# Optimization experiments

Measured on AMD Instinct MI355X. Metric: run time of the kernel, lower is better.

The kernel has to match this reference:

```python
import jax, jax.numpy as jnp
import numpy as np

N_NODES = 50000
N_EDGES = 500000
H_DIM = 128
OUT_DIM = 16
N_RELS = 90
N_BASES = 4


def setup_inputs() -> dict:
    key = jax.random.key(0)
    ks = jax.random.split(key, 12)
    inp = {
        'node_ids': jnp.arange(N_NODES, dtype=jnp.int32),
        'src': jax.random.randint(ks[0], (N_EDGES,), 0, N_NODES, dtype=jnp.int32),
        'dst': jax.random.randint(ks[1], (N_EDGES,), 0, N_NODES, dtype=jnp.int32),
        'etype': jax.random.randint(ks[2], (N_EDGES,), 0, N_RELS, dtype=jnp.int32),
        'emb': jax.random.normal(ks[3], (N_NODES, H_DIM), jnp.float32),
        'basis1': jax.random.normal(ks[4], (N_BASES, H_DIM, H_DIM), jnp.float32) * (1.0 / np.sqrt(H_DIM)),
        'comp1': jax.random.normal(ks[5], (N_RELS, N_BASES), jnp.float32) * (1.0 / np.sqrt(N_BASES)),
        'loop_w1': jax.random.normal(ks[6], (H_DIM, H_DIM), jnp.float32) * (1.0 / np.sqrt(H_DIM)),
        'bias1': jnp.zeros((H_DIM,), jnp.float32),
        'basis2': jax.random.normal(ks[7], (N_BASES, H_DIM, OUT_DIM), jnp.float32) * (1.0 / np.sqrt(H_DIM)),
        'comp2': jax.random.normal(ks[8], (N_RELS, N_BASES), jnp.float32) * (1.0 / np.sqrt(N_BASES)),
        'loop_w2': jax.random.normal(ks[9], (H_DIM, OUT_DIM), jnp.float32) * (1.0 / np.sqrt(H_DIM)),
        'bias2': jnp.zeros((OUT_DIM,), jnp.float32),
    }
    return inp


def _rel_graph_conv(x, src, dst, etype, basis, comp, loop_w, bias, num_nodes):
    # Basis decomposition: W_r = sum_b comp[r,b] * basis[b].
    # Project node features through each basis first (N is smaller than E),
    # then combine per-edge with relation coefficients: avoids per-edge GEMM.
    xb = jnp.einsum('ni,bio->nbo', x, basis)            # [N, B, out]
    msg = jnp.einsum('eb,ebo->eo', comp[etype], xb[src])  # [E, out]
    agg = jax.ops.segment_sum(msg, dst, num_segments=num_nodes)  # [N, out]
    # apply_norm=True: divide aggregated messages by in-degree of dst.
    deg = jax.ops.segment_sum(jnp.ones((src.shape[0],), x.dtype), dst,
                              num_segments=num_nodes)
    h = agg * (1.0 / jnp.maximum(deg, 1.0))[:, None]
    # self_loop=True plus bias.
    return h + x @ loop_w + bias


def reference(node_ids, src, dst, etype, emb, basis1, comp1, loop_w1, bias1,
              basis2, comp2, loop_w2, bias2):
    n = emb.shape[0]
    x = emb[node_ids]                                   # embedding lookup
    h = jax.nn.relu(_rel_graph_conv(x, src, dst, etype, basis1, comp1,
                                    loop_w1, bias1, n))
    out = _rel_graph_conv(h, src, dst, etype, basis2, comp2, loop_w2, bias2, n)
    return out
```

## Files before the change

kernel.cpp:

```cpp
#include <hip/hip_runtime.h>
#include <hip/hip_bf16.h>

#define N_NODES 50000
#define N_EDGES 500000
#define H_DIM 128
#define OUT_DIM 16
#define KDIM 640

typedef short short8 __attribute__((ext_vector_type(8)));
typedef float f32x4 __attribute__((ext_vector_type(4)));
typedef float f32x2 __attribute__((ext_vector_type(2)));

__device__ inline unsigned short f2b(float f) {
  unsigned u = __float_as_uint(f);
  u += 0x7fffu + ((u >> 16) & 1u);
  return (unsigned short)(u >> 16);
}
__device__ inline float b2f(unsigned short u) {
  return __uint_as_float(((unsigned)u) << 16);
}

__device__ __forceinline__ void gload_lds16(const unsigned short* g, unsigned short* l) {
  __builtin_amdgcn_global_load_lds(
      (const __attribute__((address_space(1))) unsigned int*)g,
      (__attribute__((address_space(3))) unsigned int*)l, 16, 0, 0);
}

#define CONV_BLOCKS 6250
#define PREP_BLOCKS 360
#define INIT_BLOCKS 196
__global__ void prologue_kernel(const int* __restrict__ node_ids, const float* __restrict__ emb,
                                unsigned short* __restrict__ Abuf,
                                const float* __restrict__ basis1, const float* __restrict__ loop_w1,
                                const float* __restrict__ basis2, const float* __restrict__ loop_w2,
                                unsigned short* __restrict__ B1t, unsigned short* __restrict__ B2pt,
                                int* __restrict__ cntA, int* __restrict__ cntB,
                                int* __restrict__ counter) {
  int b = blockIdx.x;
  if (b < CONV_BLOCKS) {
    int tid = b * 256 + threadIdx.x;
    if (tid >= N_NODES * (H_DIM / 4)) return;
    int n = tid >> 5;
    int q = tid & 31;
    int id = node_ids[n];
    const float4 v = *reinterpret_cast<const float4*>(emb + (size_t)id * H_DIM + q * 4);
    uint2 p;
    p.x = (unsigned)f2b(v.x) | ((unsigned)f2b(v.y) << 16);
    p.y = (unsigned)f2b(v.z) | ((unsigned)f2b(v.w) << 16);
    *reinterpret_cast<uint2*>(Abuf + (size_t)n * KDIM + 512 + q * 4) = p;
  } else if (b < CONV_BLOCKS + PREP_BLOCKS) {
    int tid = (b - CONV_BLOCKS) * 256 + threadIdx.x;
    if (tid < 128 * KDIM) {
      int c = tid / KDIM, k = tid % KDIM;
      float v = (k < 512) ? basis1[k * 128 + c] : loop_w1[(k - 512) * 128 + c];
      B1t[c * KDIM + k] = f2b(v);
    } else if (tid < 128 * KDIM + 80 * 128) {
      int t2 = tid - 128 * KDIM;
      int c = t2 / 128, k = t2 % 128;
      float v = (c < 64) ? basis2[(c >> 4) * 128 * 16 + k * 16 + (c & 15)]
                         : loop_w2[k * 16 + (c - 64)];
      B2pt[c * 128 + k] = f2b(v);
    }
  } else {
    int i = (b - CONV_BLOCKS - PREP_BLOCKS) * 256 + threadIdx.x;
    if (i < N_NODES) {
      cntA[i] = 0;
      cntB[i] = 0;
    }
    if (i == 0) *counter = 0;
  }
}

__global__ void count_kernel(const int* __restrict__ dst, int* __restrict__ cnt) {
  for (int e = blockIdx.x * blockDim.x + threadIdx.x; e < N_EDGES; e += gridDim.x * blockDim.x)
    atomicAdd(&cnt[dst[e]], 1);
}

__global__ void alloc_kernel(const int* __restrict__ cnt, int* __restrict__ start,
                             int* __restrict__ counter) {
  int i = blockIdx.x * blockDim.x + threadIdx.x;
  int lane = threadIdx.x & 63;
  int c = (i < N_NODES) ? cnt[i] : 0;
  int incl = c;
#pragma unroll
  for (int off = 1; off < 64; off <<= 1) {
    int v = __shfl_up(incl, off, 64);
    if (lane >= off) incl += v;
  }
  int waveTotal = __shfl(incl, 63, 64);
  int base = 0;
  if (lane == 63) base = atomicAdd(counter, waveTotal);
  base = __shfl(base, 63, 64);
  if (i < N_NODES) start[i] = base + incl - c;
}

__global__ void fill_kernel(const int* __restrict__ src, const int* __restrict__ dst,
                            const int* __restrict__ et, const int* __restrict__ csr_start,
                            int* __restrict__ cnt, unsigned* __restrict__ csr_se) {
  for (int e = blockIdx.x * blockDim.x + threadIdx.x; e < N_EDGES; e += gridDim.x * blockDim.x) {
    int d = dst[e];
    int idx = csr_start[d] + atomicAdd(&cnt[d], 1);
    csr_se[idx] = (unsigned)src[e] | ((unsigned)et[e] << 16);
  }
}

__global__ __launch_bounds__(256) void agg_kernel(const int* __restrict__ csr_start,
                                                  const int* __restrict__ csr_cnt,
                                                  const unsigned* __restrict__ csr_se,
                                                  const float* __restrict__ comp,
                                                  unsigned short* __restrict__ Abuf) {
  int node = blockIdx.x * 4 + (threadIdx.x >> 6);
  if (node >= N_NODES) return;
  int lane = threadIdx.x & 63;
  int lo = __builtin_amdgcn_readfirstlane(csr_start[node]);
  int deg = __builtin_amdgcn_readfirstlane(csr_cnt[node]);
  int hi = lo + deg;

  f32x2 a0 = {0.f, 0.f}, a1 = {0.f, 0.f}, a2 = {0.f, 0.f}, a3 = {0.f, 0.f};
  const unsigned short* featb = Abuf + 512;
  const int laneoff = lane * 2;

#define EDGE_BODY(J)                                                                   \
  {                                                                                    \
    unsigned v = __builtin_amdgcn_readlane(myse, (J));                                 \
    int s = (int)(v & 0xFFFFu);                                                        \
    int t = (int)(v >> 16);                                                            \
    unsigned u = *reinterpret_cast<const unsigned*>(featb + s * KDIM + laneoff);       \
    float4 c = *reinterpret_cast<const float4*>(comp + t * 4);                         \
    f32x2 x;                                                                           \
    x.x = __uint_as_float(u << 16);                                                    \
    x.y = __uint_as_float(u & 0xffff0000u);                                            \
    a0 = __builtin_elementwise_fma((f32x2){c.x, c.x}, x, a0);                          \
    a1 = __builtin_elementwise_fma((f32x2){c.y, c.y}, x, a1);                          \
    a2 = __builtin_elementwise_fma((f32x2){c.z, c.z}, x, a2);                          \
    a3 = __builtin_elementwise_fma((f32x2){c.w, c.w}, x, a3);                          \
  }

  for (int e0 = lo; e0 < hi; e0 += 64) {
    int nchunk = min(hi - e0, 64);
    unsigned myse = 0;
    if (e0 + lane < hi) myse = csr_se[e0 + lane];
    int j = 0;
    for (; j + 8 <= nchunk; j += 8) {
      EDGE_BODY(j)
      EDGE_BODY(j + 1)
      EDGE_BODY(j + 2)
      EDGE_BODY(j + 3)
      EDGE_BODY(j + 4)
      EDGE_BODY(j + 5)
      EDGE_BODY(j + 6)
      EDGE_BODY(j + 7)
    }
    if (j + 4 <= nchunk) {
      EDGE_BODY(j)
      EDGE_BODY(j + 1)
      EDGE_BODY(j + 2)
      EDGE_BODY(j + 3)
      j += 4;
    }
    for (; j < nchunk; ++j) { EDGE_BODY(j) }
  }
#undef EDGE_BODY

  float inv = 1.0f / (float)(deg > 0 ? deg : 1);
  unsigned short* out = Abuf + (size_t)node * KDIM;
  unsigned p0w = (unsigned)f2b(a0.x * inv) | ((unsigned)f2b(a0.y * inv) << 16);
  unsigned p1w = (unsigned)f2b(a1.x * inv) | ((unsigned)f2b(a1.y * inv) << 16);
  unsigned p2w = (unsigned)f2b(a2.x * inv) | ((unsigned)f2b(a2.y * inv) << 16);
  unsigned p3w = (unsigned)f2b(a3.x * inv) | ((unsigned)f2b(a3.y * inv) << 16);
  *reinterpret_cast<unsigned*>(out + 0 * 128 + laneoff) = p0w;
  *reinterpret_cast<unsigned*>(out + 1 * 128 + laneoff) = p1w;
  *reinterpret_cast<unsigned*>(out + 2 * 128 + laneoff) = p2w;
  *reinterpret_cast<unsigned*>(out + 3 * 128 + laneoff) = p3w;
}

__global__ __launch_bounds__(256) void agg2_kernel(const int* __restrict__ csr_start,
                                                   const int* __restrict__ csr_cnt,
                                                   const unsigned* __restrict__ csr_se,
                                                   const float* __restrict__ comp,
                                                   const unsigned short* __restrict__ Abuf,
                                                   const float* __restrict__ bias2,
                                                   float* __restrict__ dout) {
  int node = blockIdx.x * 4 + (threadIdx.x >> 6);
  if (node >= N_NODES) return;
  int lane = threadIdx.x & 63;
  int bsel = lane >> 4;
  int o = lane & 15;
  int lo = __builtin_amdgcn_readfirstlane(csr_start[node]);
  int deg = __builtin_amdgcn_readfirstlane(csr_cnt[node]);
  int hi = lo + deg;

  float acc = 0.f;

#define EDGE2_BODY(J)                                                      \
  {                                                                        \
    unsigned v = __builtin_amdgcn_readlane(myse, (J));                     \
    int s = (int)(v & 0xFFFFu);                                            \
    int t = (int)(v >> 16);                                                \
    unsigned short u = Abuf[s * KDIM + lane];                              \
    float4 c = *reinterpret_cast<const float4*>(comp + t * 4);             \
    float cb = (bsel < 2) ? ((bsel == 0) ? c.x : c.y)                      \
                          : ((bsel == 2) ? c.z : c.w);                     \
    acc = fmaf(cb, b2f(u), acc);                                           \
  }

  for (int e0 = lo; e0 < hi; e0 += 64) {
    int nchunk = min(hi - e0, 64);
    unsigned myse = 0;
    if (e0 + lane < hi) myse = csr_se[e0 + lane];
    int j = 0;
    for (; j + 8 <= nchunk; j += 8) {
      EDGE2_BODY(j)
      EDGE2_BODY(j + 1)
      EDGE2_BODY(j + 2)
      EDGE2_BODY(j + 3)
      EDGE2_BODY(j + 4)
      EDGE2_BODY(j + 5)
      EDGE2_BODY(j + 6)
      EDGE2_BODY(j + 7)
    }
    if (j + 4 <= nchunk) {
      EDGE2_BODY(j)
      EDGE2_BODY(j + 1)
      EDGE2_BODY(j + 2)
      EDGE2_BODY(j + 3)
      j += 4;
    }
    for (; j < nchunk; ++j) { EDGE2_BODY(j) }
  }
#undef EDGE2_BODY

  acc += __shfl_xor(acc, 16, 64);
  acc += __shfl_xor(acc, 32, 64);

  if (lane < 16) {
    float inv = 1.0f / (float)(deg > 0 ? deg : 1);
    float sl = b2f(Abuf[(size_t)node * KDIM + 64 + o]);
    dout[(size_t)node * OUT_DIM + o] = acc * inv + sl + bias2[o];
  }
}

__global__ __launch_bounds__(256) void gemm1p_kernel(const unsigned short* __restrict__ A,
                                                     const unsigned short* __restrict__ B1t,
                                                     const float* __restrict__ bias1,
                                                     const unsigned short* __restrict__ B2pt,
                                                     unsigned short* __restrict__ Abuf, int M) {
  __shared__ unsigned short As[64][64];
  __shared__ unsigned short Bs[128][64];
  __shared__ unsigned short Hs[64][128];
  int wave = threadIdx.x >> 6;
  int lane = threadIdx.x & 63;
  int row0 = blockIdx.x * 64;
  int kh = lane >> 4;
  int cl = lane & 15;
  int ar = wave * 16 + cl;
  f32x4 acc[8] = {};

  for (int k0 = 0; k0 < KDIM; k0 += 64) {
#pragma unroll
    for (int p = 0; p < 2; ++p) {
      int cid = threadIdx.x + p * 256;
      int r = cid >> 3, c8 = cid & 7;
      int gr = row0 + r;
      gload_lds16(A + (size_t)gr * KDIM + k0 + ((c8 ^ (r & 7)) * 8), &As[0][0] + cid * 8);
    }
#pragma unroll
    for (int p = 0; p < 4; ++p) {
      int cid = threadIdx.x + p * 256;
      int r = cid >> 3, c8 = cid & 7;
      gload_lds16(B1t + (size_t)r * KDIM + k0 + ((c8 ^ (r & 7)) * 8), &Bs[0][0] + cid * 8);
    }
    __syncthreads();
    short8 a0 = *reinterpret_cast<const short8*>(&As[ar][((kh) ^ (ar & 7)) * 8]);
    short8 a1 = *reinterpret_cast<const short8*>(&As[ar][((4 + kh) ^ (ar & 7)) * 8]);
#pragma unroll
    for (int ct = 0; ct < 8; ++ct) {
      int bc = ct * 16 + cl;
      short8 b0 = *reinterpret_cast<const short8*>(&Bs[bc][((kh) ^ (bc & 7)) * 8]);
      short8 b1 = *reinterpret_cast<const short8*>(&Bs[bc][((4 + kh) ^ (bc & 7)) * 8]);
      acc[ct] = __builtin_amdgcn_mfma_f32_16x16x32_bf16(a0, b0, acc[ct], 0, 0, 0);
      acc[ct] = __builtin_amdgcn_mfma_f32_16x16x32_bf16(a1, b1, acc[ct], 0, 0, 0);
    }
    __syncthreads();
  }

  int rb = wave * 16 + (lane >> 4) * 4;
#pragma unroll
  for (int ct = 0; ct < 8; ++ct) {
    int col = ct * 16 + cl;
    float bv = bias1[col];
#pragma unroll
    for (int r = 0; r < 4; ++r) {
      int lr = rb + r;
      float v = fmaxf(acc[ct][r] + bv, 0.0f);
      unsigned short hb = f2b(v);
      int c8 = col >> 3;
      int c8s = (c8 & 8) | ((c8 ^ lr) & 7);
      *reinterpret_cast<unsigned short*>(
          reinterpret_cast<char*>(&Hs[lr][0]) + c8s * 16 + (col & 7) * 2) = hb;
    }
  }
  __syncthreads();

  f32x4 acc2[5] = {};
  for (int k0 = 0; k0 < 128; k0 += 64) {
    for (int cid = threadIdx.x; cid < 80 * 8; cid += 256) {
      int r = cid >> 3, c8 = cid & 7;
      short8 v = *reinterpret_cast<const short8*>(B2pt + r * 128 + k0 + c8 * 8);
      *reinterpret_cast<short8*>(&Bs[r][(c8 ^ (r & 7)) * 8]) = v;
    }
    __syncthreads();
    int c8a = (k0 >> 3) + kh;
    int c8b = (k0 >> 3) + 4 + kh;
    short8 a0 = *reinterpret_cast<const short8*>(
        reinterpret_cast<char*>(&Hs[ar][0]) + (((c8a ^ ar) & 7) | (c8a & 8)) * 16);
    short8 a1 = *reinterpret_cast<const short8*>(
        reinterpret_cast<char*>(&Hs[ar][0]) + (((c8b ^ ar) & 7) | (c8b & 8)) * 16);
#pragma unroll
    for (int ct = 0; ct < 5; ++ct) {
      int bc = ct * 16 + cl;
      short8 b0 = *reinterpret_cast<const short8*>(&Bs[bc][((kh) ^ (bc & 7)) * 8]);
      short8 b1 = *reinterpret_cast<const short8*>(&Bs[bc][((4 + kh) ^ (bc & 7)) * 8]);
      acc2[ct] = __builtin_amdgcn_mfma_f32_16x16x32_bf16(a0, b0, acc2[ct], 0, 0, 0);
      acc2[ct] = __builtin_amdgcn_mfma_f32_16x16x32_bf16(a1, b1, acc2[ct], 0, 0, 0);
    }
    __syncthreads();
  }

#pragma unroll
  for (int ct = 0; ct < 5; ++ct) {
    int col = ct * 16 + cl;
#pragma unroll
    for (int r = 0; r < 4; ++r) {
      int gr = row0 + rb + r;
      if (gr < M) Abuf[(size_t)gr * KDIM + col] = f2b(acc2[ct][r]);
    }
  }
}

extern "C" void kernel_launch(void* const* d_in, const int* in_sizes, int n_in,
                              void* d_out, int out_size, void* d_ws, size_t ws_size,
                              hipStream_t stream) {
  const int* node_ids = (const int*)d_in[0];
  const int* src = (const int*)d_in[1];
  const int* dst = (const int*)d_in[2];
  const int* etype = (const int*)d_in[3];
  const float* emb = (const float*)d_in[4];
  const float* basis1 = (const float*)d_in[5];
  const float* comp1 = (const float*)d_in[6];
  const float* loop_w1 = (const float*)d_in[7];
  const float* bias1 = (const float*)d_in[8];
  const float* basis2 = (const float*)d_in[9];
  const float* comp2 = (const float*)d_in[10];
  const float* loop_w2 = (const float*)d_in[11];
  const float* bias2 = (const float*)d_in[12];
  (void)in_sizes; (void)n_in; (void)out_size; (void)ws_size;

  char* ws = (char*)d_ws;
  size_t off = 0;
  auto alloc = [&](size_t bytes) -> void* {
    void* p = ws + off;
    off += (bytes + 255) & ~(size_t)255;
    return p;
  };
  int* csr_start = (int*)alloc(N_NODES * sizeof(int));
  int* cntA = (int*)alloc(N_NODES * sizeof(int));
  int* cntB = (int*)alloc(N_NODES * sizeof(int));
  int* counter = (int*)alloc(sizeof(int));
  unsigned* csr_se = (unsigned*)alloc((size_t)N_EDGES * sizeof(unsigned));
  unsigned short* Abuf = (unsigned short*)alloc((size_t)N_NODES * KDIM * sizeof(unsigned short));
  unsigned short* B1t = (unsigned short*)alloc(128 * KDIM * sizeof(unsigned short));
  unsigned short* B2pt = (unsigned short*)alloc(80 * 128 * sizeof(unsigned short));

  prologue_kernel<<<CONV_BLOCKS + PREP_BLOCKS + INIT_BLOCKS, 256, 0, stream>>>(
      node_ids, emb, Abuf, basis1, loop_w1, basis2, loop_w2, B1t, B2pt, cntA, cntB, counter);
  count_kernel<<<1024, 256, 0, stream>>>(dst, cntA);
  alloc_kernel<<<(N_NODES + 255) / 256, 256, 0, stream>>>(cntA, csr_start, counter);
  fill_kernel<<<1024, 256, 0, stream>>>(src, dst, etype, csr_start, cntB, csr_se);

  agg_kernel<<<(N_NODES + 3) / 4, 256, 0, stream>>>(csr_start, cntA, csr_se, comp1, Abuf);
  gemm1p_kernel<<<(N_NODES + 63) / 64, 256, 0, stream>>>(Abuf, B1t, bias1, B2pt, Abuf, N_NODES);

  agg2_kernel<<<(N_NODES + 3) / 4, 256, 0, stream>>>(csr_start, cntA, csr_se, comp2, Abuf,
                                                     bias2, (float*)d_out);
}
```

Before: 146.8 us.

## Process two nodes per wave in aggregation and double-buffer GEMM LDS tiles

Both aggregation kernels now give each wavefront two consecutive destination nodes. They load the CSR start and count as int2 and prefetch the first edge chunk for both nodes up front, so the edge-record loads of the second node overlap with work on the first. The fused GEMM kernel now uses a double-buffered LDS layout: it issues async global-to-LDS loads for the next K tile while MFMAs run on the current one, and reuses one shared buffer for Hs and the second-stage B tile. The cost is fewer waves in the aggregation kernels, which gives less latency hiding across waves, and a larger LDS footprint per block in the GEMM, which may lower occupancy.

New measurement: 149.2 us. Within noise of the previous version (+1.6%).

```diff
diff --git a/kernel.cpp b/kernel.cpp
--- a/kernel.cpp
+++ b/kernel.cpp
@@ -109,14 +109,19 @@
                                                   const unsigned* __restrict__ csr_se,
                                                   const float* __restrict__ comp,
                                                   unsigned short* __restrict__ Abuf) {
-  int node = blockIdx.x * 4 + (threadIdx.x >> 6);
-  if (node >= N_NODES) return;
+  int pair = blockIdx.x * 4 + (threadIdx.x >> 6);
+  int nodeA = pair * 2;
+  if (nodeA >= N_NODES) return;
   int lane = threadIdx.x & 63;
-  int lo = __builtin_amdgcn_readfirstlane(csr_start[node]);
-  int deg = __builtin_amdgcn_readfirstlane(csr_cnt[node]);
-  int hi = lo + deg;
-
-  f32x2 a0 = {0.f, 0.f}, a1 = {0.f, 0.f}, a2 = {0.f, 0.f}, a3 = {0.f, 0.f};
+  int2 st2 = *reinterpret_cast<const int2*>(csr_start + nodeA);
+  int2 ct2 = *reinterpret_cast<const int2*>(csr_cnt + nodeA);
+  int loA = __builtin_amdgcn_readfirstlane(st2.x);
+  int degA = __builtin_amdgcn_readfirstlane(ct2.x);
+  int loB = __builtin_amdgcn_readfirstlane(st2.y);
+  int degB = __builtin_amdgcn_readfirstlane(ct2.y);
+  unsigned recA = (lane < degA) ? csr_se[loA + lane] : 0;
+  unsigned recB = (lane < degB) ? csr_se[loB + lane] : 0;
+
   const unsigned short* featb = Abuf + 512;
   const int laneoff = lane * 2;
 
@@ -136,42 +141,41 @@
     a3 = __builtin_elementwise_fma((f32x2){c.w, c.w}, x, a3);                          \
   }
 
-  for (int e0 = lo; e0 < hi; e0 += 64) {
-    int nchunk = min(hi - e0, 64);
-    unsigned myse = 0;
-    if (e0 + lane < hi) myse = csr_se[e0 + lane];
-    int j = 0;
-    for (; j + 8 <= nchunk; j += 8) {
-      EDGE_BODY(j)
-      EDGE_BODY(j + 1)
-      EDGE_BODY(j + 2)
-      EDGE_BODY(j + 3)
-      EDGE_BODY(j + 4)
-      EDGE_BODY(j + 5)
-      EDGE_BODY(j + 6)
-      EDGE_BODY(j + 7)
-    }
-    if (j + 4 <= nchunk) {
-      EDGE_BODY(j)
-      EDGE_BODY(j + 1)
-      EDGE_BODY(j + 2)
-      EDGE_BODY(j + 3)
-      j += 4;
-    }
-    for (; j < nchunk; ++j) { EDGE_BODY(j) }
-  }
+#define PROCESS1(NODE, LO, DEG, REC0)                                                  \
+  {                                                                                    \
+    f32x2 a0 = {0.f, 0.f}, a1 = {0.f, 0.f}, a2 = {0.f, 0.f}, a3 = {0.f, 0.f};          \
+    int hi = (LO) + (DEG);                                                             \
+    unsigned myse = (REC0);                                                            \
+    for (int e0 = (LO); e0 < hi; e0 += 64) {                                           \
+      int nchunk = min(hi - e0, 64);                                                   \
+      if (e0 != (LO)) myse = (e0 + lane < hi) ? csr_se[e0 + lane] : 0;                 \
+      int j = 0;                                                                       \
+      for (; j + 8 <= nchunk; j += 8) {                                                \
+        EDGE_BODY(j) EDGE_BODY(j + 1) EDGE_BODY(j + 2) EDGE_BODY(j + 3)                \
+        EDGE_BODY(j + 4) EDGE_BODY(j + 5) EDGE_BODY(j + 6) EDGE_BODY(j + 7)            \
+      }                                                                                \
+      if (j + 4 <= nchunk) {                                                           \
+        EDGE_BODY(j) EDGE_BODY(j + 1) EDGE_BODY(j + 2) EDGE_BODY(j + 3)                \
+        j += 4;                                                                        \
+      }                                                                                \
+      for (; j < nchunk; ++j) { EDGE_BODY(j) }                                         \
+    }                                                                                  \
+    float inv = 1.0f / (float)((DEG) > 0 ? (DEG) : 1);                                 \
+    unsigned short* out = Abuf + (size_t)(NODE)*KDIM;                                  \
+    unsigned p0w = (unsigned)f2b(a0.x * inv) | ((unsigned)f2b(a0.y * inv) << 16);      \
+    unsigned p1w = (unsigned)f2b(a1.x * inv) | ((unsigned)f2b(a1.y * inv) << 16);      \
+    unsigned p2w = (unsigned)f2b(a2.x * inv) | ((unsigned)f2b(a2.y * inv) << 16);      \
+    unsigned p3w = (unsigned)f2b(a3.x * inv) | ((unsigned)f2b(a3.y * inv) << 16);      \
+    *reinterpret_cast<unsigned*>(out + 0 * 128 + laneoff) = p0w;                       \
+    *reinterpret_cast<unsigned*>(out + 1 * 128 + laneoff) = p1w;                       \
+    *reinterpret_cast<unsigned*>(out + 2 * 128 + laneoff) = p2w;                       \
+    *reinterpret_cast<unsigned*>(out + 3 * 128 + laneoff) = p3w;                       \
+  }
+
+  PROCESS1(nodeA, loA, degA, recA)
+  PROCESS1(nodeA + 1, loB, degB, recB)
+#undef PROCESS1
 #undef EDGE_BODY
-
-  float inv = 1.0f / (float)(deg > 0 ? deg : 1);
-  unsigned short* out = Abuf + (size_t)node * KDIM;
-  unsigned p0w = (unsigned)f2b(a0.x * inv) | ((unsigned)f2b(a0.y * inv) << 16);
-  unsigned p1w = (unsigned)f2b(a1.x * inv) | ((unsigned)f2b(a1.y * inv) << 16);
-  unsigned p2w = (unsigned)f2b(a2.x * inv) | ((unsigned)f2b(a2.y * inv) << 16);
-  unsigned p3w = (unsigned)f2b(a3.x * inv) | ((unsigned)f2b(a3.y * inv) << 16);
-  *reinterpret_cast<unsigned*>(out + 0 * 128 + laneoff) = p0w;
-  *reinterpret_cast<unsigned*>(out + 1 * 128 + laneoff) = p1w;
-  *reinterpret_cast<unsigned*>(out + 2 * 128 + laneoff) = p2w;
-  *reinterpret_cast<unsigned*>(out + 3 * 128 + laneoff) = p3w;
 }
 
 __global__ __launch_bounds__(256) void agg2_kernel(const int* __restrict__ csr_start,
@@ -181,16 +185,20 @@
                                                    const unsigned short* __restrict__ Abuf,
                                                    const float* __restrict__ bias2,
                                                    float* __restrict__ dout) {
-  int node = blockIdx.x * 4 + (threadIdx.x >> 6);
-  if (node >= N_NODES) return;
+  int pair = blockIdx.x * 4 + (threadIdx.x >> 6);
+  int nodeA = pair * 2;
+  if (nodeA >= N_NODES) return;
   int lane = threadIdx.x & 63;
   int bsel = lane >> 4;
   int o = lane & 15;
-  int lo = __builtin_amdgcn_readfirstlane(csr_start[node]);
-  int deg = __builtin_amdgcn_readfirstlane(csr_cnt[node]);
-  int hi = lo + deg;
-
-  float acc = 0.f;
+  int2 st2 = *reinterpret_cast<const int2*>(csr_start + nodeA);
+  int2 ct2 = *reinterpret_cast<const int2*>(csr_cnt + nodeA);
+  int loA = __builtin_amdgcn_readfirstlane(st2.x);
+  int degA = __builtin_amdgcn_readfirstlane(ct2.x);
+  int loB = __builtin_amdgcn_readfirstlane(st2.y);
+  int degB = __builtin_amdgcn_readfirstlane(ct2.y);
+  unsigned recA = (lane < degA) ? csr_se[loA + lane] : 0;
+  unsigned recB = (lane < degB) ? csr_se[loB + lane] : 0;
 
 #define EDGE2_BODY(J)                                                      \
   {                                                                        \
@@ -204,40 +212,38 @@
     acc = fmaf(cb, b2f(u), acc);                                           \
   }
 
-  for (int e0 = lo; e0 < hi; e0 += 64) {
-    int nchunk = min(hi - e0, 64);
-    unsigned myse = 0;
-    if (e0 + lane < hi) myse = csr_se[e0 + lane];
-    int j = 0;
-    for (; j + 8 <= nchunk; j += 8) {
-      EDGE2_BODY(j)
-      EDGE2_BODY(j + 1)
-      EDGE2_BODY(j + 2)
-      EDGE2_BODY(j + 3)
-      EDGE2_BODY(j + 4)
-      EDGE2_BODY(j + 5)
-      EDGE2_BODY(j + 6)
-      EDGE2_BODY(j + 7)
-    }
-    if (j + 4 <= nchunk) {
-      EDGE2_BODY(j)
-      EDGE2_BODY(j + 1)
-      EDGE2_BODY(j + 2)
-      EDGE2_BODY(j + 3)
-      j += 4;
-    }
-    for (; j < nchunk; ++j) { EDGE2_BODY(j) }
-  }
+#define PROCESS2(NODE, LO, DEG, REC0)                                      \
+  {                                                                        \
+    float acc = 0.f;                                                       \
+    int hi = (LO) + (DEG);                                                 \
+    unsigned myse = (REC0);                                                \
+    for (int e0 = (LO); e0 < hi; e0 += 64) {                               \
+      int nchunk = min(hi - e0, 64);                                       \
+      if (e0 != (LO)) myse = (e0 + lane < hi) ? csr_se[e0 + lane] : 0;     \
+      int j = 0;                                                           \
+      for (; j + 8 <= nchunk; j += 8) {                                    \
+        EDGE2_BODY(j) EDGE2_BODY(j + 1) EDGE2_BODY(j + 2) EDGE2_BODY(j + 3)\
+        EDGE2_BODY(j + 4) EDGE2_BODY(j + 5) EDGE2_BODY(j + 6) EDGE2_BODY(j + 7)\
+      }                                                                    \
+      if (j + 4 <= nchunk) {                                               \
+        EDGE2_BODY(j) EDGE2_BODY(j + 1) EDGE2_BODY(j + 2) EDGE2_BODY(j + 3)\
+        j += 4;                                                            \
+      }                                                                    \
+      for (; j < nchunk; ++j) { EDGE2_BODY(j) }                            \
+    }                                                                      \
+    acc += __shfl_xor(acc, 16, 64);                                        \
+    acc += __shfl_xor(acc, 32, 64);                                        \
+    if (lane < 16) {                                                       \
+      float inv = 1.0f / (float)((DEG) > 0 ? (DEG) : 1);                   \
+      float sl = b2f(Abuf[(size_t)(NODE)*KDIM + 64 + o]);                  \
+      dout[(size_t)(NODE)*OUT_DIM + o] = acc * inv + sl + bias2[o];        \
+    }                                                                      \
+  }
+
+  PROCESS2(nodeA, loA, degA, recA)
+  PROCESS2(nodeA + 1, loB, degB, recB)
+#undef PROCESS2
 #undef EDGE2_BODY
-
-  acc += __shfl_xor(acc, 16, 64);
-  acc += __shfl_xor(acc, 32, 64);
-
-  if (lane < 16) {
-    float inv = 1.0f / (float)(deg > 0 ? deg : 1);
-    float sl = b2f(Abuf[(size_t)node * KDIM + 64 + o]);
-    dout[(size_t)node * OUT_DIM + o] = acc * inv + sl + bias2[o];
-  }
 }
 
 __global__ __launch_bounds__(256) void gemm1p_kernel(const unsigned short* __restrict__ A,
@@ -245,9 +251,11 @@
                                                      const float* __restrict__ bias1,
                                                      const unsigned short* __restrict__ B2pt,
                                                      unsigned short* __restrict__ Abuf, int M) {
-  __shared__ unsigned short As[64][64];
-  __shared__ unsigned short Bs[128][64];
-  __shared__ unsigned short Hs[64][128];
+  __shared__ unsigned short lds[24576];
+  unsigned short* AsB[2] = {lds, lds + 4096};
+  unsigned short* BsB[2] = {lds + 8192, lds + 16384};
+  unsigned short* Hs = lds;
+
   int wave = threadIdx.x >> 6;
   int lane = threadIdx.x & 63;
   int row0 = blockIdx.x * 64;
@@ -256,33 +264,43 @@
   int ar = wave * 16 + cl;
   f32x4 acc[8] = {};
 
-  for (int k0 = 0; k0 < KDIM; k0 += 64) {
-#pragma unroll
-    for (int p = 0; p < 2; ++p) {
-      int cid = threadIdx.x + p * 256;
-      int r = cid >> 3, c8 = cid & 7;
-      int gr = row0 + r;
-      gload_lds16(A + (size_t)gr * KDIM + k0 + ((c8 ^ (r & 7)) * 8), &As[0][0] + cid * 8);
-    }
-#pragma unroll
-    for (int p = 0; p < 4; ++p) {
-      int cid = threadIdx.x + p * 256;
-      int r = cid >> 3, c8 = cid & 7;
-      gload_lds16(B1t + (size_t)r * KDIM + k0 + ((c8 ^ (r & 7)) * 8), &Bs[0][0] + cid * 8);
-    }
-    __syncthreads();
-    short8 a0 = *reinterpret_cast<const short8*>(&As[ar][((kh) ^ (ar & 7)) * 8]);
-    short8 a1 = *reinterpret_cast<const short8*>(&As[ar][((4 + kh) ^ (ar & 7)) * 8]);
+#define STAGE(AP, BP, K0)                                                              \
+  {                                                                                    \
+    _Pragma("unroll") for (int p = 0; p < 2; ++p) {                                    \
+      int cid = threadIdx.x + p * 256;                                                 \
+      int r = cid >> 3, c8 = cid & 7;                                                  \
+      int gr = row0 + r;                  \
+      gload_lds16(A + (size_t)gr * KDIM + (K0) + ((c8 ^ (r & 7)) * 8), (AP) + cid * 8);\
+    }                                                                                  \
+    _Pragma("unroll") for (int p = 0; p < 4; ++p) {                                    \
+      int cid = threadIdx.x + p * 256;                                                 \
+      int r = cid >> 3, c8 = cid & 7;                                                  \
+      gload_lds16(B1t + (size_t)r * KDIM + (K0) + ((c8 ^ (r & 7)) * 8), (BP) + cid * 8);\
+    }                                                                                  \
+  }
+
+  STAGE(AsB[0], BsB[0], 0)
+  __syncthreads();
+  int cur = 0;
+#pragma unroll
+  for (int step = 0; step < KDIM / 64; ++step) {
+    if (step + 1 < KDIM / 64) STAGE(AsB[cur ^ 1], BsB[cur ^ 1], (step + 1) * 64)
+    const unsigned short* Ac = AsB[cur];
+    const unsigned short* Bc = BsB[cur];
+    short8 a0 = *reinterpret_cast<const short8*>(Ac + ar * 64 + ((kh ^ (ar & 7)) * 8));
+    short8 a1 = *reinterpret_cast<const short8*>(Ac + ar * 64 + (((4 + kh) ^ (ar & 7)) * 8));
 #pragma unroll
     for (int ct = 0; ct < 8; ++ct) {
       int bc = ct * 16 + cl;
-      short8 b0 = *reinterpret_cast<const short8*>(&Bs[bc][((kh) ^ (bc & 7)) * 8]);
-      short8 b1 = *reinterpret_cast<const short8*>(&Bs[bc][((4 + kh) ^ (bc & 7)) * 8]);
+      short8 b0 = *reinterpret_cast<const short8*>(Bc + bc * 64 + ((kh ^ (bc & 7)) * 8));
+      short8 b1 = *reinterpret_cast<const short8*>(Bc + bc * 64 + (((4 + kh) ^ (bc & 7)) * 8));
       acc[ct] = __builtin_amdgcn_mfma_f32_16x16x32_bf16(a0, b0, acc[ct], 0, 0, 0);
       acc[ct] = __builtin_amdgcn_mfma_f32_16x16x32_bf16(a1, b1, acc[ct], 0, 0, 0);
     }
     __syncthreads();
-  }
+    cur ^= 1;
+  }
+#undef STAGE
 
   int rb = wave * 16 + (lane >> 4) * 4;
 #pragma unroll
@@ -297,30 +315,31 @@
       int c8 = col >> 3;
       int c8s = (c8 & 8) | ((c8 ^ lr) & 7);
       *reinterpret_cast<unsigned short*>(
-          reinterpret_cast<char*>(&Hs[lr][0]) + c8s * 16 + (col & 7) * 2) = hb;
+          reinterpret_cast<char*>(Hs + lr * 128) + c8s * 16 + (col & 7) * 2) = hb;
     }
   }
   __syncthreads();
 
+  unsigned short* Bp = BsB[0];
   f32x4 acc2[5] = {};
   for (int k0 = 0; k0 < 128; k0 += 64) {
     for (int cid = threadIdx.x; cid < 80 * 8; cid += 256) {
       int r = cid >> 3, c8 = cid & 7;
       short8 v = *reinterpret_cast<const short8*>(B2pt + r * 128 + k0 + c8 * 8);
-      *reinterpret_cast<short8*>(&Bs[r][(c8 ^ (r & 7)) * 8]) = v;
+      *reinterpret_cast<short8*>(Bp + r * 64 + (c8 ^ (r & 7)) * 8) = v;
     }
     __syncthreads();
     int c8a = (k0 >> 3) + kh;
     int c8b = (k0 >> 3) + 4 + kh;
     short8 a0 = *reinterpret_cast<const short8*>(
-        reinterpret_cast<char*>(&Hs[ar][0]) + (((c8a ^ ar) & 7) | (c8a & 8)) * 16);
+        reinterpret_cast<char*>(Hs + ar * 128) + (((c8a ^ ar) & 7) | (c8a & 8)) * 16);
     short8 a1 = *reinterpret_cast<const short8*>(
-        reinterpret_cast<char*>(&Hs[ar][0]) + (((c8b ^ ar) & 7) | (c8b & 8)) * 16);
+        reinterpret_cast<char*>(Hs + ar * 128) + (((c8b ^ ar) & 7) | (c8b & 8)) * 16);
 #pragma unroll
     for (int ct = 0; ct < 5; ++ct) {
       int bc = ct * 16 + cl;
-      short8 b0 = *reinterpret_cast<const short8*>(&Bs[bc][((kh) ^ (bc & 7)) * 8]);
-      short8 b1 = *reinterpret_cast<const short8*>(&Bs[bc][((4 + kh) ^ (bc & 7)) * 8]);
+      short8 b0 = *reinterpret_cast<const short8*>(Bp + bc * 64 + ((kh ^ (bc & 7)) * 8));
+      short8 b1 = *reinterpret_cast<const short8*>(Bp + bc * 64 + (((4 + kh) ^ (bc & 7)) * 8));
       acc2[ct] = __builtin_amdgcn_mfma_f32_16x16x32_bf16(a0, b0, acc2[ct], 0, 0, 0);
       acc2[ct] = __builtin_amdgcn_mfma_f32_16x16x32_bf16(a1, b1, acc2[ct], 0, 0, 0);
     }
@@ -378,9 +397,9 @@
   alloc_kernel<<<(N_NODES + 255) / 256, 256, 0, stream>>>(cntA, csr_start, counter);
   fill_kernel<<<1024, 256, 0, stream>>>(src, dst, etype, csr_start, cntB, csr_se);
 
-  agg_kernel<<<(N_NODES + 3) / 4, 256, 0, stream>>>(csr_start, cntA, csr_se, comp1, Abuf);
+  agg_kernel<<<(N_NODES / 2 + 3) / 4, 256, 0, stream>>>(csr_start, cntA, csr_se, comp1, Abuf);
   gemm1p_kernel<<<(N_NODES + 63) / 64, 256, 0, stream>>>(Abuf, B1t, bias1, B2pt, Abuf, N_NODES);
 
-  agg2_kernel<<<(N_NODES + 3) / 4, 256, 0, stream>>>(csr_start, cntA, csr_se, comp2, Abuf,
-                                                     bias2, (float*)d_out);
-}
+  agg2_kernel<<<(N_NODES / 2 + 3) / 4, 256, 0, stream>>>(csr_start, cntA, csr_se, comp2, Abuf,
+                                                         bias2, (float*)d_out);
+}
```

## Fuse layer-1 edge aggregation into the GEMM kernel via LDS staging

Applied to the files above, without the earlier changes.

The per-node aggregation kernel and the layer-1 GEMM kernel are merged into one kernel. Each wave aggregates 16 destination nodes in turn, prefetching the next node's edge records, and writes the aggregated bf16 rows into a swizzled LDS tile rather than to global memory. The GEMM then reads its A operand from LDS, with the self-loop features loaded straight into registers. This removes the global write and re-read of the large intermediate buffer and one kernel launch, but uses about 80KB of LDS per block, which sharply reduces how many waves can hide gather latency during aggregation.

Measured after the change: 171.0 us. 16.4% more time.

```diff
diff --git a/kernel.cpp b/kernel.cpp
--- a/kernel.cpp
+++ b/kernel.cpp
@@ -104,21 +104,54 @@
   }
 }
 
-__global__ __launch_bounds__(256) void agg_kernel(const int* __restrict__ csr_start,
-                                                  const int* __restrict__ csr_cnt,
-                                                  const unsigned* __restrict__ csr_se,
-                                                  const float* __restrict__ comp,
-                                                  unsigned short* __restrict__ Abuf) {
-  int node = blockIdx.x * 4 + (threadIdx.x >> 6);
-  if (node >= N_NODES) return;
+__device__ __forceinline__ int swzA(int r, int c) {
+  return r * 512 + (c >> 6) * 64 + ((((c >> 3) & 7) ^ (r & 7)) * 8) + (c & 7);
+}
+
+__global__ __launch_bounds__(256) void agemm_kernel(const int* __restrict__ csr_start,
+                                                    const int* __restrict__ csr_cnt,
+                                                    const unsigned* __restrict__ csr_se,
+                                                    const float* __restrict__ comp,
+                                                    const unsigned short* __restrict__ B1t,
+                                                    const float* __restrict__ bias1,
+                                                    const unsigned short* __restrict__ B2pt,
+                                                    unsigned short* __restrict__ Abuf, int M) {
+  __shared__ unsigned short lds[64 * 512 + 128 * 64];
+  unsigned short* Ys = lds;
+  unsigned short* Bs = lds + 64 * 512;
+  unsigned short* Hs = lds;
+
+  int wave = threadIdx.x >> 6;
   int lane = threadIdx.x & 63;
-  int lo = __builtin_amdgcn_readfirstlane(csr_start[node]);
-  int deg = __builtin_amdgcn_readfirstlane(csr_cnt[node]);
-  int hi = lo + deg;
-
-  f32x2 a0 = {0.f, 0.f}, a1 = {0.f, 0.f}, a2 = {0.f, 0.f}, a3 = {0.f, 0.f};
+  int row0 = blockIdx.x * 64;
+  int kh = lane >> 4;
+  int cl = lane & 15;
+  int ar = wave * 16 + cl;
+
+#pragma unroll
+  for (int p = 0; p < 4; ++p) {
+    int cid = threadIdx.x + p * 256;
+    int r = cid >> 3, c8 = cid & 7;
+    gload_lds16(B1t + (size_t)r * KDIM + ((c8 ^ (r & 7)) * 8), Bs + cid * 8);
+  }
+
+  const unsigned short* xrow = Abuf + (size_t)(row0 + ar) * KDIM + 512;
+  short8 xa0 = *reinterpret_cast<const short8*>(xrow + kh * 8);
+  short8 xa1 = *reinterpret_cast<const short8*>(xrow + 32 + kh * 8);
+  short8 xa2 = *reinterpret_cast<const short8*>(xrow + 64 + kh * 8);
+  short8 xa3 = *reinterpret_cast<const short8*>(xrow + 96 + kh * 8);
+
+  int nodeBase = row0 + wave * 16;
+  bool mv = (lane < 16) && (nodeBase + lane < M);
+  int mst = mv ? csr_start[nodeBase + lane] : 0;
+  int mct = mv ? csr_cnt[nodeBase + lane] : 0;
+
   const unsigned short* featb = Abuf + 512;
   const int laneoff = lane * 2;
+
+  int loCur = __builtin_amdgcn_readlane(mst, 0);
+  int degCur = __builtin_amdgcn_readlane(mct, 0);
+  unsigned recCur = (lane < degCur) ? csr_se[loCur + lane] : 0;
 
 #define EDGE_BODY(J)                                                                   \
   {                                                                                    \
@@ -136,42 +169,133 @@
     a3 = __builtin_elementwise_fma((f32x2){c.w, c.w}, x, a3);                          \
   }
 
-  for (int e0 = lo; e0 < hi; e0 += 64) {
-    int nchunk = min(hi - e0, 64);
-    unsigned myse = 0;
-    if (e0 + lane < hi) myse = csr_se[e0 + lane];
-    int j = 0;
-    for (; j + 8 <= nchunk; j += 8) {
-      EDGE_BODY(j)
-      EDGE_BODY(j + 1)
-      EDGE_BODY(j + 2)
-      EDGE_BODY(j + 3)
-      EDGE_BODY(j + 4)
-      EDGE_BODY(j + 5)
-      EDGE_BODY(j + 6)
-      EDGE_BODY(j + 7)
-    }
-    if (j + 4 <= nchunk) {
-      EDGE_BODY(j)
-      EDGE_BODY(j + 1)
-      EDGE_BODY(j + 2)
-      EDGE_BODY(j + 3)
-      j += 4;
-    }
-    for (; j < nchunk; ++j) { EDGE_BODY(j) }
+  for (int i = 0; i < 16; ++i) {
+    int loNext = 0, degNext = 0;
+    unsigned recNext = 0;
+    if (i < 15) {
+      loNext = __builtin_amdgcn_readlane(mst, i + 1);
+      degNext = __builtin_amdgcn_readlane(mct, i + 1);
+      recNext = (lane < degNext) ? csr_se[loNext + lane] : 0;
+    }
+    f32x2 a0 = {0.f, 0.f}, a1 = {0.f, 0.f}, a2 = {0.f, 0.f}, a3 = {0.f, 0.f};
+    int hi = loCur + degCur;
+    unsigned myse = recCur;
+    for (int e0 = loCur; e0 < hi; e0 += 64) {
+      int nchunk = min(hi - e0, 64);
+      if (e0 != loCur) myse = (e0 + lane < hi) ? csr_se[e0 + lane] : 0;
+      int j = 0;
+      for (; j + 8 <= nchunk; j += 8) {
+        EDGE_BODY(j) EDGE_BODY(j + 1) EDGE_BODY(j + 2) EDGE_BODY(j + 3)
+        EDGE_BODY(j + 4) EDGE_BODY(j + 5) EDGE_BODY(j + 6) EDGE_BODY(j + 7)
+      }
+      if (j + 4 <= nchunk) {
+        EDGE_BODY(j) EDGE_BODY(j + 1) EDGE_BODY(j + 2) EDGE_BODY(j + 3)
+        j += 4;
+      }
+      for (; j < nchunk; ++j) { EDGE_BODY(j) }
+    }
+    float inv = 1.0f / (float)(degCur > 0 ? degCur : 1);
+    int r = wave * 16 + i;
+    unsigned w0 = (unsigned)f2b(a0.x * inv) | ((unsigned)f2b(a0.y * inv) << 16);
+    unsigned w1 = (unsigned)f2b(a1.x * inv) | ((unsigned)f2b(a1.y * inv) << 16);
+    unsigned w2 = (unsigned)f2b(a2.x * inv) | ((unsigned)f2b(a2.y * inv) << 16);
+    unsigned w3 = (unsigned)f2b(a3.x * inv) | ((unsigned)f2b(a3.y * inv) << 16);
+    *reinterpret_cast<unsigned*>(Ys + swzA(r, 0 * 128 + laneoff)) = w0;
+    *reinterpret_cast<unsigned*>(Ys + swzA(r, 1 * 128 + laneoff)) = w1;
+    *reinterpret_cast<unsigned*>(Ys + swzA(r, 2 * 128 + laneoff)) = w2;
+    *reinterpret_cast<unsigned*>(Ys + swzA(r, 3 * 128 + laneoff)) = w3;
+    loCur = loNext;
+    degCur = degNext;
+    recCur = recNext;
   }
 #undef EDGE_BODY
 
-  float inv = 1.0f / (float)(deg > 0 ? deg : 1);
-  unsigned short* out = Abuf + (size_t)node * KDIM;
-  unsigned p0w = (unsigned)f2b(a0.x * inv) | ((unsigned)f2b(a0.y * inv) << 16);
-  unsigned p1w = (unsigned)f2b(a1.x * inv) | ((unsigned)f2b(a1.y * inv) << 16);
-  unsigned p2w = (unsigned)f2b(a2.x * inv) | ((unsigned)f2b(a2.y * inv) << 16);
-  unsigned p3w = (unsigned)f2b(a3.x * inv) | ((unsigned)f2b(a3.y * inv) << 16);
-  *reinterpret_cast<unsigned*>(out + 0 * 128 + laneoff) = p0w;
-  *reinterpret_cast<unsigned*>(out + 1 * 128 + laneoff) = p1w;
-  *reinterpret_cast<unsigned*>(out + 2 * 128 + laneoff) = p2w;
-  *reinterpret_cast<unsigned*>(out + 3 * 128 + laneoff) = p3w;
+  f32x4 acc[8] = {};
+#pragma unroll
+  for (int g = 0; g < 10; ++g) {
+    if (g > 0) {
+#pragma unroll
+      for (int p = 0; p < 4; ++p) {
+        int cid = threadIdx.x + p * 256;
+        int r = cid >> 3, c8 = cid & 7;
+        gload_lds16(B1t + (size_t)r * KDIM + g * 64 + ((c8 ^ (r & 7)) * 8), Bs + cid * 8);
+      }
+    }
+    __syncthreads();
+    short8 a0, a1;
+    if (g < 8) {
+      a0 = *reinterpret_cast<const short8*>(Ys + swzA(ar, g * 64 + kh * 8));
+      a1 = *reinterpret_cast<const short8*>(Ys + swzA(ar, g * 64 + 32 + kh * 8));
+    } else if (g == 8) {
+      a0 = xa0;
+      a1 = xa1;
+    } else {
+      a0 = xa2;
+      a1 = xa3;
+    }
+#pragma unroll
+    for (int ct = 0; ct < 8; ++ct) {
+      int bc = ct * 16 + cl;
+      short8 b0 = *reinterpret_cast<const short8*>(Bs + bc * 64 + ((kh ^ (bc & 7)) * 8));
+      short8 b1 = *reinterpret_cast<const short8*>(Bs + bc * 64 + (((4 + kh) ^ (bc & 7)) * 8));
+      acc[ct] = __builtin_amdgcn_mfma_f32_16x16x32_bf16(a0, b0, acc[ct], 0, 0, 0);
+      acc[ct] = __builtin_amdgcn_mfma_f32_16x16x32_bf16(a1, b1, acc[ct], 0, 0, 0);
+    }
+    __syncthreads();
+  }
+
+  int rb = wave * 16 + (lane >> 4) * 4;
+#pragma unroll
+  for (int ct = 0; ct < 8; ++ct) {
+    int col = ct * 16 + cl;
+    float bv = bias1[col];
+#pragma unroll
+    for (int r = 0; r < 4; ++r) {
+      int lr = rb + r;
+      float v = fmaxf(acc[ct][r] + bv, 0.0f);
+      unsigned short hb = f2b(v);
+      int c8 = col >> 3;
+      int c8s = (c8 & 8) | ((c8 ^ lr) & 7);
+      *reinterpret_cast<unsigned short*>(
+          reinterpret_cast<char*>(Hs + lr * 128) + c8s * 16 + (col & 7) * 2) = hb;
+    }
+  }
+  __syncthreads();
+
+  f32x4 acc2[5] = {};
+  for (int k0 = 0; k0 < 128; k0 += 64) {
+    for (int cid = threadIdx.x; cid < 80 * 8; cid += 256) {
+      int r = cid >> 3, c8 = cid & 7;
+      short8 v = *reinterpret_cast<const short8*>(B2pt + r * 128 + k0 + c8 * 8);
+      *reinterpret_cast<short8*>(Bs + r * 64 + (c8 ^ (r & 7)) * 8) = v;
+    }
+    __syncthreads();
+    int c8a = (k0 >> 3) + kh;
+    int c8b = (k0 >> 3) + 4 + kh;
+    short8 a0 = *reinterpret_cast<const short8*>(
+        reinterpret_cast<char*>(Hs + ar * 128) + (((c8a ^ ar) & 7) | (c8a & 8)) * 16);
+    short8 a1 = *reinterpret_cast<const short8*>(
+        reinterpret_cast<char*>(Hs + ar * 128) + (((c8b ^ ar) & 7) | (c8b & 8)) * 16);
+#pragma unroll
+    for (int ct = 0; ct < 5; ++ct) {
+      int bc = ct * 16 + cl;
+      short8 b0 = *reinterpret_cast<const short8*>(Bs + bc * 64 + ((kh ^ (bc & 7)) * 8));
+      short8 b1 = *reinterpret_cast<const short8*>(Bs + bc * 64 + (((4 + kh) ^ (bc & 7)) * 8));
+      acc2[ct] = __builtin_amdgcn_mfma_f32_16x16x32_bf16(a0, b0, acc2[ct], 0, 0, 0);
+      acc2[ct] = __builtin_amdgcn_mfma_f32_16x16x32_bf16(a1, b1, acc2[ct], 0, 0, 0);
+    }
+    __syncthreads();
+  }
+
+#pragma unroll
+  for (int ct = 0; ct < 5; ++ct) {
+    int col = ct * 16 + cl;
+#pragma unroll
+    for (int r = 0; r < 4; ++r) {
+      int gr = row0 + rb + r;
+      if (gr < M) Abuf[(size_t)gr * KDIM + col] = f2b(acc2[ct][r]);
+    }
+  }
 }
 
 __global__ __launch_bounds__(256) void agg2_kernel(const int* __restrict__ csr_start,
@@ -237,104 +361,6 @@
     float inv = 1.0f / (float)(deg > 0 ? deg : 1);
     float sl = b2f(Abuf[(size_t)node * KDIM + 64 + o]);
     dout[(size_t)node * OUT_DIM + o] = acc * inv + sl + bias2[o];
-  }
-}
-
-__global__ __launch_bounds__(256) void gemm1p_kernel(const unsigned short* __restrict__ A,
-                                                     const unsigned short* __restrict__ B1t,
-                                                     const float* __restrict__ bias1,
-                                                     const unsigned short* __restrict__ B2pt,
-                                                     unsigned short* __restrict__ Abuf, int M) {
-  __shared__ unsigned short As[64][64];
-  __shared__ unsigned short Bs[128][64];
-  __shared__ unsigned short Hs[64][128];
-  int wave = threadIdx.x >> 6;
-  int lane = threadIdx.x & 63;
-  int row0 = blockIdx.x * 64;
-  int kh = lane >> 4;
-  int cl = lane & 15;
-  int ar = wave * 16 + cl;
-  f32x4 acc[8] = {};
-
-  for (int k0 = 0; k0 < KDIM; k0 += 64) {
-#pragma unroll
-    for (int p = 0; p < 2; ++p) {
-      int cid = threadIdx.x + p * 256;
-      int r = cid >> 3, c8 = cid & 7;
-      int gr = row0 + r;
-      gload_lds16(A + (size_t)gr * KDIM + k0 + ((c8 ^ (r & 7)) * 8), &As[0][0] + cid * 8);
-    }
-#pragma unroll
-    for (int p = 0; p < 4; ++p) {
-      int cid = threadIdx.x + p * 256;
-      int r = cid >> 3, c8 = cid & 7;
-      gload_lds16(B1t + (size_t)r * KDIM + k0 + ((c8 ^ (r & 7)) * 8), &Bs[0][0] + cid * 8);
-    }
-    __syncthreads();
-    short8 a0 = *reinterpret_cast<const short8*>(&As[ar][((kh) ^ (ar & 7)) * 8]);
-    short8 a1 = *reinterpret_cast<const short8*>(&As[ar][((4 + kh) ^ (ar & 7)) * 8]);
-#pragma unroll
-    for (int ct = 0; ct < 8; ++ct) {
-      int bc = ct * 16 + cl;
-      short8 b0 = *reinterpret_cast<const short8*>(&Bs[bc][((kh) ^ (bc & 7)) * 8]);
-      short8 b1 = *reinterpret_cast<const short8*>(&Bs[bc][((4 + kh) ^ (bc & 7)) * 8]);
-      acc[ct] = __builtin_amdgcn_mfma_f32_16x16x32_bf16(a0, b0, acc[ct], 0, 0, 0);
-      acc[ct] = __builtin_amdgcn_mfma_f32_16x16x32_bf16(a1, b1, acc[ct], 0, 0, 0);
-    }
-    __syncthreads();
-  }
-
-  int rb = wave * 16 + (lane >> 4) * 4;
-#pragma unroll
-  for (int ct = 0; ct < 8; ++ct) {
-    int col = ct * 16 + cl;
-    float bv = bias1[col];
-#pragma unroll
-    for (int r = 0; r < 4; ++r) {
-      int lr = rb + r;
-      float v = fmaxf(acc[ct][r] + bv, 0.0f);
-      unsigned short hb = f2b(v);
-      int c8 = col >> 3;
-      int c8s = (c8 & 8) | ((c8 ^ lr) & 7);
-      *reinterpret_cast<unsigned short*>(
-          reinterpret_cast<char*>(&Hs[lr][0]) + c8s * 16 + (col & 7) * 2) = hb;
-    }
-  }
-  __syncthreads();
-
-  f32x4 acc2[5] = {};
-  for (int k0 = 0; k0 < 128; k0 += 64) {
-    for (int cid = threadIdx.x; cid < 80 * 8; cid += 256) {
-      int r = cid >> 3, c8 = cid & 7;
-      short8 v = *reinterpret_cast<const short8*>(B2pt + r * 128 + k0 + c8 * 8);
-      *reinterpret_cast<short8*>(&Bs[r][(c8 ^ (r & 7)) * 8]) = v;
-    }
-    __syncthreads();
-    int c8a = (k0 >> 3) + kh;
-    int c8b = (k0 >> 3) + 4 + kh;
-    short8 a0 = *reinterpret_cast<const short8*>(
-        reinterpret_cast<char*>(&Hs[ar][0]) + (((c8a ^ ar) & 7) | (c8a & 8)) * 16);
-    short8 a1 = *reinterpret_cast<const short8*>(
-        reinterpret_cast<char*>(&Hs[ar][0]) + (((c8b ^ ar) & 7) | (c8b & 8)) * 16);
-#pragma unroll
-    for (int ct = 0; ct < 5; ++ct) {
-      int bc = ct * 16 + cl;
-      short8 b0 = *reinterpret_cast<const short8*>(&Bs[bc][((kh) ^ (bc & 7)) * 8]);
-      short8 b1 = *reinterpret_cast<const short8*>(&Bs[bc][((4 + kh) ^ (bc & 7)) * 8]);
-      acc2[ct] = __builtin_amdgcn_mfma_f32_16x16x32_bf16(a0, b0, acc2[ct], 0, 0, 0);
-      acc2[ct] = __builtin_amdgcn_mfma_f32_16x16x32_bf16(a1, b1, acc2[ct], 0, 0, 0);
-    }
-    __syncthreads();
-  }
-
-#pragma unroll
-  for (int ct = 0; ct < 5; ++ct) {
-    int col = ct * 16 + cl;
-#pragma unroll
-    for (int r = 0; r < 4; ++r) {
-      int gr = row0 + rb + r;
-      if (gr < M) Abuf[(size_t)gr * KDIM + col] = f2b(acc2[ct][r]);
-    }
   }
 }
 
@@ -378,8 +404,8 @@
   alloc_kernel<<<(N_NODES + 255) / 256, 256, 0, stream>>>(cntA, csr_start, counter);
   fill_kernel<<<1024, 256, 0, stream>>>(src, dst, etype, csr_start, cntB, csr_se);
 
-  agg_kernel<<<(N_NODES + 3) / 4, 256, 0, stream>>>(csr_start, cntA, csr_se, comp1, Abuf);
-  gemm1p_kernel<<<(N_NODES + 63) / 64, 256, 0, stream>>>(Abuf, B1t, bias1, B2pt, Abuf, N_NODES);
+  agemm_kernel<<<(N_NODES + 63) / 64, 256, 0, stream>>>(csr_start, cntA, csr_se, comp1, B1t,
+                                                        bias1, B2pt, Abuf, N_NODES);
 
   agg2_kernel<<<(N_NODES + 3) / 4, 256, 0, stream>>>(csr_start, cntA, csr_se, comp2, Abuf,
                                                      bias2, (float*)d_out);
```

## Double-buffer B tiles and load A fragments directly to registers in gemm1p

Applied to the files above, without the earlier changes.

The first GEMM in gemm1p now double-buffers the B1t tile in LDS, prefetching the next k-slice while MFMAs run on the current one, and drops the per-step barrier that waited for loads to land. A fragments are read straight from global memory into registers, with the next slice prefetched one step ahead, instead of being staged through LDS. LDS is unified into one 32KB buffer aliased between the B buffers and the H tile, which lowers LDS use per block and may allow more blocks per CU. The risk is that the global_load_lds prefetch for the next buffer relies on the single end-of-step barrier for ordering, and the direct A loads may be less coalesced than the old LDS staging.

New measurement: 148.8 us. No clear change (+1.4%).

```diff
diff --git a/kernel.cpp b/kernel.cpp
--- a/kernel.cpp
+++ b/kernel.cpp
@@ -245,9 +245,10 @@
                                                      const float* __restrict__ bias1,
                                                      const unsigned short* __restrict__ B2pt,
                                                      unsigned short* __restrict__ Abuf, int M) {
-  __shared__ unsigned short As[64][64];
-  __shared__ unsigned short Bs[128][64];
-  __shared__ unsigned short Hs[64][128];
+  __shared__ unsigned short lds[16384];
+  unsigned short* BsB[2] = {lds, lds + 8192};
+  unsigned short* Hs = lds;
+
   int wave = threadIdx.x >> 6;
   int lane = threadIdx.x & 63;
   int row0 = blockIdx.x * 64;
@@ -256,33 +257,44 @@
   int ar = wave * 16 + cl;
   f32x4 acc[8] = {};
 
-  for (int k0 = 0; k0 < KDIM; k0 += 64) {
-#pragma unroll
-    for (int p = 0; p < 2; ++p) {
-      int cid = threadIdx.x + p * 256;
-      int r = cid >> 3, c8 = cid & 7;
-      int gr = row0 + r;
-      gload_lds16(A + (size_t)gr * KDIM + k0 + ((c8 ^ (r & 7)) * 8), &As[0][0] + cid * 8);
-    }
-#pragma unroll
-    for (int p = 0; p < 4; ++p) {
-      int cid = threadIdx.x + p * 256;
-      int r = cid >> 3, c8 = cid & 7;
-      gload_lds16(B1t + (size_t)r * KDIM + k0 + ((c8 ^ (r & 7)) * 8), &Bs[0][0] + cid * 8);
-    }
-    __syncthreads();
-    short8 a0 = *reinterpret_cast<const short8*>(&As[ar][((kh) ^ (ar & 7)) * 8]);
-    short8 a1 = *reinterpret_cast<const short8*>(&As[ar][((4 + kh) ^ (ar & 7)) * 8]);
+  const unsigned short* Arow = A + (size_t)(row0 + ar) * KDIM;
+
+#define STAGE_B(BP, K0)                                                                 \
+  {                                                                                     \
+    _Pragma("unroll") for (int p = 0; p < 4; ++p) {                                     \
+      int cid = threadIdx.x + p * 256;                                                  \
+      int r = cid >> 3, c8 = cid & 7;                                                   \
+      gload_lds16(B1t + (size_t)r * KDIM + (K0) + ((c8 ^ (r & 7)) * 8), (BP) + cid * 8);\
+    }                                                                                   \
+  }
+
+  short8 a0 = *reinterpret_cast<const short8*>(Arow + kh * 8);
+  short8 a1 = *reinterpret_cast<const short8*>(Arow + 32 + kh * 8);
+  STAGE_B(BsB[0], 0)
+  __syncthreads();
+
+#pragma unroll
+  for (int step = 0; step < 10; ++step) {
+    short8 na0, na1;
+    if (step < 9) {
+      na0 = *reinterpret_cast<const short8*>(Arow + (step + 1) * 64 + kh * 8);
+      na1 = *reinterpret_cast<const short8*>(Arow + (step + 1) * 64 + 32 + kh * 8);
+      STAGE_B(BsB[(step + 1) & 1], (step + 1) * 64)
+    }
+    const unsigned short* Bc = BsB[step & 1];
 #pragma unroll
     for (int ct = 0; ct < 8; ++ct) {
       int bc = ct * 16 + cl;
-      short8 b0 = *reinterpret_cast<const short8*>(&Bs[bc][((kh) ^ (bc & 7)) * 8]);
-      short8 b1 = *reinterpret_cast<const short8*>(&Bs[bc][((4 + kh) ^ (bc & 7)) * 8]);
+      short8 b0 = *reinterpret_cast<const short8*>(Bc + bc * 64 + ((kh ^ (bc & 7)) * 8));
+      short8 b1 = *reinterpret_cast<const short8*>(Bc + bc * 64 + (((4 + kh) ^ (bc & 7)) * 8));
       acc[ct] = __builtin_amdgcn_mfma_f32_16x16x32_bf16(a0, b0, acc[ct], 0, 0, 0);
       acc[ct] = __builtin_amdgcn_mfma_f32_16x16x32_bf16(a1, b1, acc[ct], 0, 0, 0);
     }
     __syncthreads();
-  }
+    a0 = na0;
+    a1 = na1;
+  }
+#undef STAGE_B
 
   int rb = wave * 16 + (lane >> 4) * 4;
 #pragma unroll
@@ -297,32 +309,33 @@
       int c8 = col >> 3;
       int c8s = (c8 & 8) | ((c8 ^ lr) & 7);
       *reinterpret_cast<unsigned short*>(
-          reinterpret_cast<char*>(&Hs[lr][0]) + c8s * 16 + (col & 7) * 2) = hb;
+          reinterpret_cast<char*>(Hs + lr * 128) + c8s * 16 + (col & 7) * 2) = hb;
     }
   }
   __syncthreads();
 
+  unsigned short* Bp = BsB[1];
   f32x4 acc2[5] = {};
   for (int k0 = 0; k0 < 128; k0 += 64) {
     for (int cid = threadIdx.x; cid < 80 * 8; cid += 256) {
       int r = cid >> 3, c8 = cid & 7;
       short8 v = *reinterpret_cast<const short8*>(B2pt + r * 128 + k0 + c8 * 8);
-      *reinterpret_cast<short8*>(&Bs[r][(c8 ^ (r & 7)) * 8]) = v;
+      *reinterpret_cast<short8*>(Bp + r * 64 + (c8 ^ (r & 7)) * 8) = v;
     }
     __syncthreads();
     int c8a = (k0 >> 3) + kh;
     int c8b = (k0 >> 3) + 4 + kh;
-    short8 a0 = *reinterpret_cast<const short8*>(
-        reinterpret_cast<char*>(&Hs[ar][0]) + (((c8a ^ ar) & 7) | (c8a & 8)) * 16);
-    short8 a1 = *reinterpret_cast<const short8*>(
-        reinterpret_cast<char*>(&Hs[ar][0]) + (((c8b ^ ar) & 7) | (c8b & 8)) * 16);
+    short8 h0 = *reinterpret_cast<const short8*>(
+        reinterpret_cast<char*>(Hs + ar * 128) + (((c8a ^ ar) & 7) | (c8a & 8)) * 16);
+    short8 h1 = *reinterpret_cast<const short8*>(
+        reinterpret_cast<char*>(Hs + ar * 128) + (((c8b ^ ar) & 7) | (c8b & 8)) * 16);
 #pragma unroll
     for (int ct = 0; ct < 5; ++ct) {
       int bc = ct * 16 + cl;
-      short8 b0 = *reinterpret_cast<const short8*>(&Bs[bc][((kh) ^ (bc & 7)) * 8]);
-      short8 b1 = *reinterpret_cast<const short8*>(&Bs[bc][((4 + kh) ^ (bc & 7)) * 8]);
-      acc2[ct] = __builtin_amdgcn_mfma_f32_16x16x32_bf16(a0, b0, acc2[ct], 0, 0, 0);
-      acc2[ct] = __builtin_amdgcn_mfma_f32_16x16x32_bf16(a1, b1, acc2[ct], 0, 0, 0);
+      short8 b0 = *reinterpret_cast<const short8*>(Bp + bc * 64 + ((kh ^ (bc & 7)) * 8));
+      short8 b1 = *reinterpret_cast<const short8*>(Bp + bc * 64 + (((4 + kh) ^ (bc & 7)) * 8));
+      acc2[ct] = __builtin_amdgcn_mfma_f32_16x16x32_bf16(h0, b0, acc2[ct], 0, 0, 0);
+      acc2[ct] = __builtin_amdgcn_mfma_f32_16x16x32_bf16(h1, b1, acc2[ct], 0, 0, 0);
     }
     __syncthreads();
   }
```
